# Kernel optimization log

Measured on AMD Instinct MI355X. Metric: run time of the kernel, lower is better.

Reference implementation:

```python
import jax, jax.numpy as jnp
import numpy as np

N_NODES = 50000
N_EDGES = 300000
NODE_DIM = 11
EDGE_DIM = 5
HID = 256
L = 4
G = 1024  # num graphs
BN_EPS = 1e-5


def setup_inputs() -> dict:
    key = jax.random.key(0)
    ks = jax.random.split(key, 24)
    s = 0.05
    inp = {
        "x": jax.random.normal(ks[0], (N_NODES, NODE_DIM), jnp.float32),
        "edge_index": jax.random.randint(ks[1], (2, N_EDGES), 0, N_NODES, jnp.int32),
        "edge_attr": jax.random.normal(ks[2], (N_EDGES, EDGE_DIM), jnp.float32),
        "batch": jnp.sort(jax.random.randint(ks[3], (N_NODES,), 0, G, jnp.int32)),
        # node encoder
        "enc_W": jax.random.normal(ks[4], (NODE_DIM, HID), jnp.float32) * s,
        "enc_b": jnp.zeros((HID,), jnp.float32),
        # per-layer GINE params (stacked over layers)
        "edge_W": jax.random.normal(ks[5], (L, EDGE_DIM, HID), jnp.float32) * s,
        "edge_b": jnp.zeros((L, HID), jnp.float32),
        "mlp_W1": jax.random.normal(ks[6], (L, HID, HID), jnp.float32) * s,
        "mlp_b1": jnp.zeros((L, HID), jnp.float32),
        "mlp_W2": jax.random.normal(ks[7], (L, HID, HID), jnp.float32) * s,
        "mlp_b2": jnp.zeros((L, HID), jnp.float32),
        "bn_g": jnp.ones((L, HID), jnp.float32),
        "bn_b": jnp.zeros((L, HID), jnp.float32),
        # head: 3*HID -> HID -> HID//2 -> 1
        "head_W1": jax.random.normal(ks[8], (3 * HID, HID), jnp.float32) * s,
        "head_b1": jnp.zeros((HID,), jnp.float32),
        "head_W2": jax.random.normal(ks[9], (HID, HID // 2), jnp.float32) * s,
        "head_b2": jnp.zeros((HID // 2,), jnp.float32),
        "head_W3": jax.random.normal(ks[10], (HID // 2, 1), jnp.float32) * s,
        "head_b3": jnp.zeros((1,), jnp.float32),
    }
    return inp


def _forward(x, edge_attr, enc_W, enc_b, edge_W, edge_b, mlp_W1, mlp_b1,
             mlp_W2, mlp_b2, bn_g, bn_b, head_W1, head_b1, head_W2, head_b2,
             head_W3, head_b3, edge_index, batch):
    n = x.shape[0]
    src, dst = edge_index[0], edge_index[1]  # messages flow src(j) -> dst(i)
    h = jax.nn.relu(x @ enc_W + enc_b)  # [N, HID]
    for l in range(L):
        e = edge_attr @ edge_W[l] + edge_b[l]                 # [E, HID]
        msg = jax.nn.relu(h[src] + e)                         # [E, HID]
        aggr = jax.ops.segment_sum(msg, dst, num_segments=n)  # [N, HID]
        z = h + aggr                                          # (1+eps)*h + aggr, eps=0
        z = jax.nn.relu(z @ mlp_W1[l] + mlp_b1[l]) @ mlp_W2[l] + mlp_b2[l]
        # BatchNorm over node dim (batch statistics)
        mu = jnp.mean(z, axis=0)
        var = jnp.var(z, axis=0)
        z = (z - mu) * jax.lax.rsqrt(var + BN_EPS) * bn_g[l] + bn_b[l]
        h = jax.nn.relu(z) + h  # residual
    # mean / add / max pooling per graph
    sums = jax.ops.segment_sum(h, batch, num_segments=G)      # [G, HID]
    cnt = jax.ops.segment_sum(jnp.ones((n, 1), h.dtype), batch, num_segments=G)
    mean = sums / jnp.maximum(cnt, 1.0)
    mx = jax.ops.segment_max(h, batch, num_segments=G)
    g = jnp.concatenate([mean, sums, mx], axis=1)             # [G, 3*HID]
    g = jax.nn.relu(g @ head_W1 + head_b1)
    g = jax.nn.relu(g @ head_W2 + head_b2)
    out = g @ head_W3 + head_b3
    return out.reshape(-1)  # [G]


def reference(x, edge_index, edge_attr, batch, enc_W, enc_b, edge_W, edge_b,
              mlp_W1, mlp_b1, mlp_W2, mlp_b2, bn_g, bn_b, head_W1, head_b1,
              head_W2, head_b2, head_W3, head_b3):
    return _forward(x, edge_attr, enc_W, enc_b, edge_W, edge_b, mlp_W1, mlp_b1,
                    mlp_W2, mlp_b2, bn_g, bn_b, head_W1, head_b1, head_W2,
                    head_b2, head_W3, head_b3, edge_index, batch)
```

## Files before the change

### kernel.cpp

```cpp
#include <hip/hip_runtime.h>

#define N_NODES 50000
#define N_EDGES 300000
#define G_GRAPHS 1024
#define HID 256
#define NLAYERS 4

typedef unsigned short ushort_t;
typedef __attribute__((ext_vector_type(8))) short bf16x8;
typedef __attribute__((ext_vector_type(8))) unsigned short u16x8;
typedef __attribute__((ext_vector_type(4))) float f32x4;

__device__ __forceinline__ float bf2f(ushort_t u) {
  unsigned int x = ((unsigned int)u) << 16;
  return __builtin_bit_cast(float, x);
}
__device__ __forceinline__ ushort_t f2bf(float f) {
  unsigned int x = __builtin_bit_cast(unsigned int, f);
  unsigned int lsb = (x >> 16) & 1u;
  x += 0x7fffu + lsb;
  return (ushort_t)(x >> 16);
}

__global__ __launch_bounds__(256) void k_encoder(const float* __restrict__ x,
    const float* __restrict__ W, const float* __restrict__ b,
    ushort_t* __restrict__ h, int n)
{
  int j = threadIdx.x;
  float wcol[11];
#pragma unroll
  for (int k = 0; k < 11; ++k) wcol[k] = W[k * HID + j];
  float bj = b[j];
  __shared__ float xs[8][11];
  int base = blockIdx.x * 8;
  if (j < 88) {
    int r = j / 11, k = j % 11;
    int row = base + r;
    if (row < n) xs[r][k] = x[row * 11 + k];
  }
  __syncthreads();
#pragma unroll
  for (int r = 0; r < 8; ++r) {
    int row = base + r;
    if (row >= n) break;
    float acc = bj;
#pragma unroll
    for (int k = 0; k < 11; ++k) acc += xs[r][k] * wcol[k];
    h[(size_t)row * HID + j] = f2bf(fmaxf(acc, 0.f));
  }
}

__global__ __launch_bounds__(256) void k_hist(const int* __restrict__ dst,
    int* __restrict__ offs, int E)
{
  int e = blockIdx.x * 256 + threadIdx.x;
  if (e < E) atomicAdd(&offs[dst[e]], 1);
}

__global__ __launch_bounds__(1024) void k_scanA(int* __restrict__ offs,
    int* __restrict__ btot, int n)
{
  __shared__ int wsum[16];
  int tid = threadIdx.x, lane = tid & 63, wid = tid >> 6;
  int idx = blockIdx.x * 1024 + tid;
  int v = (idx < n) ? offs[idx] : 0;
  int x = v;
#pragma unroll
  for (int off = 1; off < 64; off <<= 1) {
    int t = __shfl_up(x, off);
    if (lane >= off) x += t;
  }
  if (lane == 63) wsum[wid] = x;
  __syncthreads();
  if (wid == 0 && lane < 16) {
    int w = wsum[lane];
#pragma unroll
    for (int off = 1; off < 16; off <<= 1) {
      int t = __shfl_up(w, off);
      if (lane >= off) w += t;
    }
    wsum[lane] = w;
  }
  __syncthreads();
  int wbase = (wid == 0) ? 0 : wsum[wid - 1];
  if (idx < n) offs[idx] = wbase + x - v;
  if (tid == 0) btot[blockIdx.x] = wsum[15];
}

__global__ __launch_bounds__(1024) void k_scanC(int* __restrict__ offs,
    const int* __restrict__ btot, int n)
{
  __shared__ int sbase;
  if (threadIdx.x == 0) {
    int s = 0;
    for (int i = 0; i < blockIdx.x; ++i) s += btot[i];
    sbase = s;
  }
  __syncthreads();
  int idx = blockIdx.x * 1024 + threadIdx.x;
  if (idx < n) offs[idx] += sbase;
}

__global__ __launch_bounds__(256) void k_fill(const int* __restrict__ src,
    const int* __restrict__ dst, int* __restrict__ offs,
    int* __restrict__ esrc, ushort_t* __restrict__ eab,
    const float* __restrict__ ea, int E)
{
  int e = blockIdx.x * 256 + threadIdx.x;
  if (e < E) {
    int d = dst[e];
    int p = atomicAdd(&offs[d], 1);
    esrc[p] = src[e];
    const float* ep = ea + (size_t)e * 5;
    ushort4 lo = make_ushort4(f2bf(ep[0]), f2bf(ep[1]), f2bf(ep[2]), f2bf(ep[3]));
    ushort4 hi = make_ushort4(f2bf(ep[4]), 0, 0, 0);
    *(ushort4*)&eab[(size_t)p * 8] = lo;
    *(ushort4*)&eab[(size_t)p * 8 + 4] = hi;
  }
}

__global__ __launch_bounds__(256) void k_prep(const float* __restrict__ W1,
    const float* __restrict__ W2, ushort_t* __restrict__ Wt1,
    ushort_t* __restrict__ Wt2)
{
  __shared__ float ld[16][257];
  int mat = blockIdx.y & (NLAYERS - 1);
  int which = blockIdx.y >> 2;
  const float* Wm = (which ? W2 : W1) + (size_t)mat * HID * HID;
  ushort_t* Wtm = (which ? Wt2 : Wt1) + (size_t)mat * HID * HID;
  int k0 = blockIdx.x * 16;
  int tid = threadIdx.x;
#pragma unroll
  for (int i = 0; i < 16; ++i) ld[i][tid] = Wm[(size_t)(k0 + i) * HID + tid];
  __syncthreads();
#pragma unroll
  for (int v = 0; v < 4; ++v) {
    ushort4 u = make_ushort4(f2bf(ld[v*4+0][tid]), f2bf(ld[v*4+1][tid]),
                             f2bf(ld[v*4+2][tid]), f2bf(ld[v*4+3][tid]));
    *(ushort4*)&Wtm[(size_t)tid * HID + k0 + v * 4] = u;
  }
}

__global__ __launch_bounds__(256) void k_prept(const float* __restrict__ W,
    ushort_t* __restrict__ Wt, int K, int N)
{
  int idx = blockIdx.x * 256 + threadIdx.x;
  if (idx >= K * N) return;
  int n = idx / K, k = idx % K;
  Wt[idx] = f2bf(W[(size_t)k * N + n]);
}

struct ev5 { ushort_t s0, s1, s2, s3, s4; };

__device__ __forceinline__ void edge_step(ev5 ev, ushort4 hv,
    const float4& w0, const float4& w1, const float4& w2, const float4& w3,
    const float4& w4, const float4& bi,
    float& ax, float& ay, float& az, float& aw)
{
  float v0 = bf2f(ev.s0), v1 = bf2f(ev.s1), v2 = bf2f(ev.s2),
        v3 = bf2f(ev.s3), v4 = bf2f(ev.s4);
  float m0 = bi.x, m1 = bi.y, m2 = bi.z, m3 = bi.w;
  m0 = fmaf(v0, w0.x, m0); m1 = fmaf(v0, w0.y, m1);
  m2 = fmaf(v0, w0.z, m2); m3 = fmaf(v0, w0.w, m3);
  m0 = fmaf(v1, w1.x, m0); m1 = fmaf(v1, w1.y, m1);
  m2 = fmaf(v1, w1.z, m2); m3 = fmaf(v1, w1.w, m3);
  m0 = fmaf(v2, w2.x, m0); m1 = fmaf(v2, w2.y, m1);
  m2 = fmaf(v2, w2.z, m2); m3 = fmaf(v2, w2.w, m3);
  m0 = fmaf(v3, w3.x, m0); m1 = fmaf(v3, w3.y, m1);
  m2 = fmaf(v3, w3.z, m2); m3 = fmaf(v3, w3.w, m3);
  m0 = fmaf(v4, w4.x, m0); m1 = fmaf(v4, w4.y, m1);
  m2 = fmaf(v4, w4.z, m2); m3 = fmaf(v4, w4.w, m3);
  m0 += bf2f(hv.x); m1 += bf2f(hv.y); m2 += bf2f(hv.z); m3 += bf2f(hv.w);
  ax += fmaxf(m0, 0.f); ay += fmaxf(m1, 0.f);
  az += fmaxf(m2, 0.f); aw += fmaxf(m3, 0.f);
}

__global__ __launch_bounds__(256) void k_gather(const ushort_t* __restrict__ h,
    const int* __restrict__ offs, const int* __restrict__ esrc,
    const ushort_t* __restrict__ eab, const float* __restrict__ eW,
    const float* __restrict__ eb, ushort_t* __restrict__ zin,
    float* __restrict__ stats, int n)
{
  int tid = threadIdx.x;
  if (blockIdx.x == 0) { stats[tid] = 0.f; stats[HID + tid] = 0.f; }
  int wave = tid >> 6, lane = tid & 63;
  int node = blockIdx.x * 4 + wave;
  int c4 = lane * 4;
  float4 w0 = *(const float4*)&eW[0 * HID + c4];
  float4 w1 = *(const float4*)&eW[1 * HID + c4];
  float4 w2 = *(const float4*)&eW[2 * HID + c4];
  float4 w3 = *(const float4*)&eW[3 * HID + c4];
  float4 w4 = *(const float4*)&eW[4 * HID + c4];
  float4 bi = *(const float4*)&eb[c4];
  if (node >= n) return;
  int lo = (node == 0) ? 0 : offs[node - 1];
  int hi = offs[node];
  ushort4 ho = *(const ushort4*)&h[(size_t)node * HID + c4];
  float ax = bf2f(ho.x), ay = bf2f(ho.y), az = bf2f(ho.z), aw = bf2f(ho.w);
  int p = lo;
  for (; p + 3 < hi; p += 4) {
    int s0 = esrc[p], s1 = esrc[p + 1], s2 = esrc[p + 2], s3 = esrc[p + 3];
    ev5 ea0 = *(const ev5*)&eab[(size_t)(p + 0) * 8];
    ev5 ea1 = *(const ev5*)&eab[(size_t)(p + 1) * 8];
    ev5 ea2 = *(const ev5*)&eab[(size_t)(p + 2) * 8];
    ev5 ea3 = *(const ev5*)&eab[(size_t)(p + 3) * 8];
    ushort4 h0 = *(const ushort4*)&h[(size_t)s0 * HID + c4];
    ushort4 h1 = *(const ushort4*)&h[(size_t)s1 * HID + c4];
    ushort4 h2 = *(const ushort4*)&h[(size_t)s2 * HID + c4];
    ushort4 h3 = *(const ushort4*)&h[(size_t)s3 * HID + c4];
    edge_step(ea0, h0, w0, w1, w2, w3, w4, bi, ax, ay, az, aw);
    edge_step(ea1, h1, w0, w1, w2, w3, w4, bi, ax, ay, az, aw);
    edge_step(ea2, h2, w0, w1, w2, w3, w4, bi, ax, ay, az, aw);
    edge_step(ea3, h3, w0, w1, w2, w3, w4, bi, ax, ay, az, aw);
  }
  for (; p < hi; ++p) {
    int s0 = esrc[p];
    ev5 ea0 = *(const ev5*)&eab[(size_t)p * 8];
    ushort4 h0 = *(const ushort4*)&h[(size_t)s0 * HID + c4];
    edge_step(ea0, h0, w0, w1, w2, w3, w4, bi, ax, ay, az, aw);
  }
  *(ushort4*)&zin[(size_t)node * HID + c4] =
      make_ushort4(f2bf(ax), f2bf(ay), f2bf(az), f2bf(aw));
}

__global__ __launch_bounds__(512, 1) void k_mlp(const ushort_t* __restrict__ A,
    const ushort_t* __restrict__ Wt1, const float* __restrict__ b1,
    const ushort_t* __restrict__ Wt2, const float* __restrict__ b2,
    ushort_t* __restrict__ out, float* __restrict__ stats, int M)
{
  __shared__ alignas(16) ushort_t z1s[2][16 * 264];
  int tid = threadIdx.x;
  int wave = tid >> 6, lane = tid & 63;
  int m = lane & 15, quad = lane >> 4;
  int col0 = wave * 32;
  bf16x8 w1f[2][8];
  bf16x8 w2f[2][8];
#pragma unroll
  for (int ct = 0; ct < 2; ++ct)
#pragma unroll
    for (int kt = 0; kt < 8; ++kt) {
      w1f[ct][kt] = *(const bf16x8*)(
          Wt1 + (size_t)(col0 + ct * 16 + m) * HID + kt * 32 + quad * 8);
      w2f[ct][kt] = *(const bf16x8*)(
          Wt2 + (size_t)(col0 + ct * 16 + m) * HID + kt * 32 + quad * 8);
    }
  float bv1[2] = {b1[col0 + m], b1[col0 + 16 + m]};
  float bv2[2] = {b2[col0 + m], b2[col0 + 16 + m]};
  float csum[2] = {0.f, 0.f}, csq[2] = {0.f, 0.f};
  int ntiles = M >> 4;
  int parity = 0;
  int t = blockIdx.x;
  bf16x8 af[8];
  if (t < ntiles) {
    const ushort_t* Ap = A + (size_t)(t * 16 + m) * HID + quad * 8;
#pragma unroll
    for (int kt = 0; kt < 8; ++kt) af[kt] = *(const bf16x8*)(Ap + kt * 32);
  }
  for (; t < ntiles; t += gridDim.x) {
    int tn = t + gridDim.x;
    int tcl = (tn < ntiles) ? tn : t;
    const ushort_t* Apn = A + (size_t)(tcl * 16 + m) * HID + quad * 8;
    bf16x8 afn[8];
#pragma unroll
    for (int kt = 0; kt < 8; ++kt) afn[kt] = *(const bf16x8*)(Apn + kt * 32);
    f32x4 a0 = (f32x4){0.f, 0.f, 0.f, 0.f};
    f32x4 a1 = (f32x4){0.f, 0.f, 0.f, 0.f};
#pragma unroll
    for (int kt = 0; kt < 8; ++kt) {
      a0 = __builtin_amdgcn_mfma_f32_16x16x32_bf16(af[kt], w1f[0][kt], a0, 0, 0, 0);
      a1 = __builtin_amdgcn_mfma_f32_16x16x32_bf16(af[kt], w1f[1][kt], a1, 0, 0, 0);
    }
    ushort_t* buf = z1s[parity];
#pragma unroll
    for (int reg = 0; reg < 4; ++reg) {
      int r = quad * 4 + reg;
      buf[r * 264 + col0 + m]      = f2bf(fmaxf(a0[reg] + bv1[0], 0.f));
      buf[r * 264 + col0 + 16 + m] = f2bf(fmaxf(a1[reg] + bv1[1], 0.f));
    }
    asm volatile("s_waitcnt lgkmcnt(0)" ::: "memory");
    __builtin_amdgcn_s_barrier();
    __builtin_amdgcn_sched_barrier(0);
    f32x4 c0 = (f32x4){0.f, 0.f, 0.f, 0.f};
    f32x4 c1 = (f32x4){0.f, 0.f, 0.f, 0.f};
#pragma unroll
    for (int kt = 0; kt < 8; ++kt) {
      bf16x8 zf = *(const bf16x8*)&buf[m * 264 + kt * 32 + quad * 8];
      c0 = __builtin_amdgcn_mfma_f32_16x16x32_bf16(zf, w2f[0][kt], c0, 0, 0, 0);
      c1 = __builtin_amdgcn_mfma_f32_16x16x32_bf16(zf, w2f[1][kt], c1, 0, 0, 0);
    }
    int rb = t * 16 + quad * 4;
#pragma unroll
    for (int reg = 0; reg < 4; ++reg) {
      float o0 = c0[reg] + bv2[0];
      float o1 = c1[reg] + bv2[1];
      out[(size_t)(rb + reg) * HID + col0 + m] = f2bf(o0);
      out[(size_t)(rb + reg) * HID + col0 + 16 + m] = f2bf(o1);
      csum[0] += o0; csq[0] = fmaf(o0, o0, csq[0]);
      csum[1] += o1; csq[1] = fmaf(o1, o1, csq[1]);
    }
#pragma unroll
    for (int kt = 0; kt < 8; ++kt) af[kt] = afn[kt];
    parity ^= 1;
  }
#pragma unroll
  for (int ct = 0; ct < 2; ++ct) {
    float s = csum[ct], q = csq[ct];
    s += __shfl_xor(s, 16); s += __shfl_xor(s, 32);
    q += __shfl_xor(q, 16); q += __shfl_xor(q, 32);
    if (quad == 0) {
      unsafeAtomicAdd(&stats[col0 + ct * 16 + m], s);
      unsafeAtomicAdd(&stats[HID + col0 + ct * 16 + m], q);
    }
  }
}

__global__ __launch_bounds__(256) void k_bn_apply(const ushort_t* __restrict__ z,
    const float* __restrict__ stats, const float* __restrict__ g,
    const float* __restrict__ b, ushort_t* __restrict__ h, int total4)
{
  int idx = blockIdx.x * 256 + threadIdx.x;
  if (idx >= total4) return;
  int col = (idx & 63) * 4;
  const float inv_n = 1.f / (float)N_NODES;
  float sc[4], sh[4];
#pragma unroll
  for (int c = 0; c < 4; ++c) {
    float mu = stats[col + c] * inv_n;
    float var = stats[HID + col + c] * inv_n - mu * mu;
    float rs = rsqrtf(var + 1e-5f);
    sc[c] = g[col + c] * rs;
    sh[c] = b[col + c] - mu * sc[c];
  }
  ushort4 zv = *(const ushort4*)(z + (size_t)idx * 4);
  ushort4 hv = *(const ushort4*)(h + (size_t)idx * 4);
  float o0 = fmaxf(fmaf(bf2f(zv.x), sc[0], sh[0]), 0.f) + bf2f(hv.x);
  float o1 = fmaxf(fmaf(bf2f(zv.y), sc[1], sh[1]), 0.f) + bf2f(hv.y);
  float o2 = fmaxf(fmaf(bf2f(zv.z), sc[2], sh[2]), 0.f) + bf2f(hv.z);
  float o3 = fmaxf(fmaf(bf2f(zv.w), sc[3], sh[3]), 0.f) + bf2f(hv.w);
  *(ushort4*)(h + (size_t)idx * 4) = make_ushort4(f2bf(o0), f2bf(o1), f2bf(o2), f2bf(o3));
}

__device__ __forceinline__ int lbound(const int* __restrict__ b, int n, int key) {
  int lo = 0, hi = n;
  while (lo < hi) {
    int mid = (lo + hi) >> 1;
    if (b[mid] < key) lo = mid + 1; else hi = mid;
  }
  return lo;
}

__global__ __launch_bounds__(256) void k_pool_bn(const ushort_t* __restrict__ z,
    const float* __restrict__ stats, const float* __restrict__ g_,
    const float* __restrict__ b_, const ushort_t* __restrict__ h,
    const int* __restrict__ batch, ushort_t* __restrict__ gf)
{
  int g = blockIdx.x, j = threadIdx.x;
  const float inv_n = 1.f / (float)N_NODES;
  float mu = stats[j] * inv_n;
  float var = stats[HID + j] * inv_n - mu * mu;
  float rs = rsqrtf(var + 1e-5f);
  float sc = g_[j] * rs;
  float sh = b_[j] - mu * sc;
  int lo = lbound(batch, N_NODES, g);
  int hi = lbound(batch, N_NODES, g + 1);
  float s = 0.f, mx = 0.f;
  for (int i = lo; i < hi; ++i) {
    float zv = bf2f(z[(size_t)i * HID + j]);
    float hv = bf2f(h[(size_t)i * HID + j]);
    float v = fmaxf(fmaf(zv, sc, sh), 0.f) + hv;
    s += v; mx = fmaxf(mx, v);
  }
  float cntv = fmaxf((float)(hi - lo), 1.f);
  size_t base = (size_t)g * 768;
  gf[base + j] = f2bf(s / cntv);
  gf[base + 256 + j] = f2bf(s);
  gf[base + 512 + j] = f2bf(mx);
}

template<int KT, int DO_RELU>
__global__ __launch_bounds__(256, 1) void k_head_gemm(const ushort_t* __restrict__ A,
    const ushort_t* __restrict__ Bt, const float* __restrict__ bias,
    ushort_t* __restrict__ out, int M, int N)
{
  const int K = KT * 32;
  int tid = threadIdx.x;
  int wave = tid >> 6, lane = tid & 63;
  int m = lane & 15, quad = lane >> 4;
  int col = (blockIdx.y * 4 + wave) * 16 + m;
  bf16x8 bfrag[KT];
#pragma unroll
  for (int kt = 0; kt < KT; ++kt)
    bfrag[kt] = *(const bf16x8*)(Bt + (size_t)col * K + kt * 32 + quad * 8);
  float bv = bias[col];
  int ntiles = M >> 4;
  for (int t = blockIdx.x; t < ntiles; t += gridDim.x) {
    const ushort_t* Ap = A + (size_t)(t * 16 + m) * K + quad * 8;
    bf16x8 af[KT];
#pragma unroll
    for (int kt = 0; kt < KT; ++kt) af[kt] = *(const bf16x8*)(Ap + kt * 32);
    f32x4 acc = (f32x4){0.f, 0.f, 0.f, 0.f};
#pragma unroll
    for (int kt = 0; kt < KT; ++kt)
      acc = __builtin_amdgcn_mfma_f32_16x16x32_bf16(af[kt], bfrag[kt], acc, 0, 0, 0);
    int rb = t * 16 + quad * 4;
#pragma unroll
    for (int reg = 0; reg < 4; ++reg) {
      float o = acc[reg] + bv;
      if (DO_RELU) o = fmaxf(o, 0.f);
      out[(size_t)(rb + reg) * N + col] = f2bf(o);
    }
  }
}

__global__ __launch_bounds__(256) void k_head_out(const ushort_t* __restrict__ g2,
    const float* __restrict__ W3, const float* __restrict__ b3,
    float* __restrict__ out)
{
  int wave = threadIdx.x >> 6, lane = threadIdx.x & 63;
  int g = blockIdx.x * 4 + wave;
  ushort2 v = *(const ushort2*)&g2[(size_t)g * 128 + lane * 2];
  float p = bf2f(v.x) * W3[lane * 2] + bf2f(v.y) * W3[lane * 2 + 1];
#pragma unroll
  for (int off = 32; off > 0; off >>= 1) p += __shfl_down(p, off);
  if (lane == 0) out[g] = p + b3[0];
}

extern "C" void kernel_launch(void* const* d_in, const int* in_sizes, int n_in,
                              void* d_out, int out_size, void* d_ws, size_t ws_size,
                              hipStream_t stream)
{
  const float* x     = (const float*)d_in[0];
  const int*   ei    = (const int*)d_in[1];
  const float* ea    = (const float*)d_in[2];
  const int*   batch = (const int*)d_in[3];
  const float* encW  = (const float*)d_in[4];
  const float* encB  = (const float*)d_in[5];
  const float* edgeW = (const float*)d_in[6];
  const float* edgeB = (const float*)d_in[7];
  const float* W1    = (const float*)d_in[8];
  const float* b1    = (const float*)d_in[9];
  const float* W2    = (const float*)d_in[10];
  const float* b2    = (const float*)d_in[11];
  const float* bng   = (const float*)d_in[12];
  const float* bnb   = (const float*)d_in[13];
  const float* hW1   = (const float*)d_in[14];
  const float* hb1   = (const float*)d_in[15];
  const float* hW2   = (const float*)d_in[16];
  const float* hb2   = (const float*)d_in[17];
  const float* hW3   = (const float*)d_in[18];
  const float* hb3   = (const float*)d_in[19];
  float* out = (float*)d_out;

  const size_t NH = (size_t)N_NODES * HID;
  char* base = (char*)d_ws;
  auto alloc = [&](size_t bytes) -> char* {
    char* p = base; base += (bytes + 63) & ~(size_t)63; return p;
  };
  float*    stats = (float*)alloc(512 * 4);
  int*      offs  = (int*)alloc(50001 * 4);
  int*      btot  = (int*)alloc(64 * 4);
  int*      esrc  = (int*)alloc((size_t)N_EDGES * 4);
  ushort_t* eab   = (ushort_t*)alloc((size_t)N_EDGES * 8 * 2);
  ushort_t* Wt1   = (ushort_t*)alloc((size_t)NLAYERS * HID * HID * 2);
  ushort_t* Wt2   = (ushort_t*)alloc((size_t)NLAYERS * HID * HID * 2);
  ushort_t* hW1t  = (ushort_t*)alloc((size_t)768 * 256 * 2);
  ushort_t* hW2t  = (ushort_t*)alloc((size_t)256 * 128 * 2);
  ushort_t* gf    = (ushort_t*)alloc((size_t)G_GRAPHS * 768 * 2);
  ushort_t* g1    = (ushort_t*)alloc((size_t)G_GRAPHS * 256 * 2);
  ushort_t* g2    = (ushort_t*)alloc((size_t)G_GRAPHS * 128 * 2);
  ushort_t* zin   = (ushort_t*)alloc(NH * 2);
  ushort_t* h     = (ushort_t*)alloc(NH * 2);

  const int* src = ei;
  const int* dst = ei + N_EDGES;

  hipMemsetAsync(offs, 0, 50001 * sizeof(int), stream);
  k_hist<<<(N_EDGES + 255) / 256, 256, 0, stream>>>(dst, offs, N_EDGES);
  const int NSB = (N_NODES + 1023) / 1024;
  k_scanA<<<NSB, 1024, 0, stream>>>(offs, btot, N_NODES);
  k_scanC<<<NSB, 1024, 0, stream>>>(offs, btot, N_NODES);
  k_fill<<<(N_EDGES + 255) / 256, 256, 0, stream>>>(src, dst, offs, esrc, eab, ea, N_EDGES);
  k_prep<<<dim3(16, 2 * NLAYERS), 256, 0, stream>>>(W1, W2, Wt1, Wt2);
  k_prept<<<(768 * 256 + 255) / 256, 256, 0, stream>>>(hW1, hW1t, 768, 256);
  k_prept<<<(256 * 128 + 255) / 256, 256, 0, stream>>>(hW2, hW2t, 256, 128);

  k_encoder<<<(N_NODES + 7) / 8, 256, 0, stream>>>(x, encW, encB, h, N_NODES);

  for (int l = 0; l < NLAYERS; ++l) {
    k_gather<<<N_NODES / 4, 256, 0, stream>>>(
        h, offs, esrc, eab, edgeW + (size_t)l * 5 * HID, edgeB + (size_t)l * HID,
        zin, stats, N_NODES);
    k_mlp<<<256, 512, 0, stream>>>(
        zin, Wt1 + (size_t)l * HID * HID, b1 + (size_t)l * HID,
        Wt2 + (size_t)l * HID * HID, b2 + (size_t)l * HID, zin, stats, N_NODES);
    if (l < NLAYERS - 1) {
      k_bn_apply<<<(N_NODES * HID / 4 + 255) / 256, 256, 0, stream>>>(
          zin, stats, bng + (size_t)l * HID, bnb + (size_t)l * HID, h,
          N_NODES * HID / 4);
    }
  }

  k_pool_bn<<<G_GRAPHS, 256, 0, stream>>>(
      zin, stats, bng + (size_t)(NLAYERS - 1) * HID,
      bnb + (size_t)(NLAYERS - 1) * HID, h, batch, gf);
  k_head_gemm<24, 1><<<dim3(16, 4), 256, 0, stream>>>(gf, hW1t, hb1, g1, G_GRAPHS, 256);
  k_head_gemm<8, 1><<<dim3(16, 2), 256, 0, stream>>>(g1, hW2t, hb2, g2, G_GRAPHS, 128);
  k_head_out<<<G_GRAPHS / 4, 256, 0, stream>>>(g2, hW3, hb3, out);
}
```

Before: 602.9 us.

## Pad CSR segments to multiples of four and pipeline gather over four-node groups

```diff
diff --git a/kernel.cpp b/kernel.cpp
--- a/kernel.cpp
+++ b/kernel.cpp
@@ -5,6 +5,7 @@
 #define G_GRAPHS 1024
 #define HID 256
 #define NLAYERS 4
+#define PAD_SLOTS (N_EDGES + 3 * N_NODES + 64)
 
 typedef unsigned short ushort_t;
 typedef __attribute__((ext_vector_type(8))) short bf16x8;
@@ -63,7 +64,8 @@
   __shared__ int wsum[16];
   int tid = threadIdx.x, lane = tid & 63, wid = tid >> 6;
   int idx = blockIdx.x * 1024 + tid;
-  int v = (idx < n) ? offs[idx] : 0;
+  int cnt = (idx < n) ? offs[idx] : 0;
+  int v = (cnt + 3) & ~3;
   int x = v;
 #pragma unroll
   for (int off = 1; off < 64; off <<= 1) {
@@ -88,17 +90,22 @@
 }
 
 __global__ __launch_bounds__(1024) void k_scanC(int* __restrict__ offs,
-    const int* __restrict__ btot, int n)
+    int* __restrict__ pstart, const int* __restrict__ btot, int n)
 {
   __shared__ int sbase;
   if (threadIdx.x == 0) {
     int s = 0;
-    for (int i = 0; i < blockIdx.x; ++i) s += btot[i];
+    for (int i = 0; i < (int)blockIdx.x; ++i) s += btot[i];
     sbase = s;
+    if (blockIdx.x == gridDim.x - 1) pstart[n] = s + btot[blockIdx.x];
   }
   __syncthreads();
   int idx = blockIdx.x * 1024 + threadIdx.x;
-  if (idx < n) offs[idx] += sbase;
+  if (idx < n) {
+    int v = offs[idx] + sbase;
+    offs[idx] = v;
+    pstart[idx] = v;
+  }
 }
 
 __global__ __launch_bounds__(256) void k_fill(const int* __restrict__ src,
@@ -113,7 +120,7 @@
     esrc[p] = src[e];
     const float* ep = ea + (size_t)e * 5;
     ushort4 lo = make_ushort4(f2bf(ep[0]), f2bf(ep[1]), f2bf(ep[2]), f2bf(ep[3]));
-    ushort4 hi = make_ushort4(f2bf(ep[4]), 0, 0, 0);
+    ushort4 hi = make_ushort4(f2bf(ep[4]), (ushort_t)0x3f80u, 0, 0);
     *(ushort4*)&eab[(size_t)p * 8] = lo;
     *(ushort4*)&eab[(size_t)p * 8 + 4] = hi;
   }
@@ -150,15 +157,14 @@
   Wt[idx] = f2bf(W[(size_t)k * N + n]);
 }
 
-struct ev5 { ushort_t s0, s1, s2, s3, s4; };
-
-__device__ __forceinline__ void edge_step(ev5 ev, ushort4 hv,
+__device__ __forceinline__ void edge_step(bf16x8 ev, ushort4 hv,
     const float4& w0, const float4& w1, const float4& w2, const float4& w3,
     const float4& w4, const float4& bi,
     float& ax, float& ay, float& az, float& aw)
 {
-  float v0 = bf2f(ev.s0), v1 = bf2f(ev.s1), v2 = bf2f(ev.s2),
-        v3 = bf2f(ev.s3), v4 = bf2f(ev.s4);
+  float v0 = bf2f((ushort_t)ev[0]), v1 = bf2f((ushort_t)ev[1]),
+        v2 = bf2f((ushort_t)ev[2]), v3 = bf2f((ushort_t)ev[3]),
+        v4 = bf2f((ushort_t)ev[4]), fl = bf2f((ushort_t)ev[5]);
   float m0 = bi.x, m1 = bi.y, m2 = bi.z, m3 = bi.w;
   m0 = fmaf(v0, w0.x, m0); m1 = fmaf(v0, w0.y, m1);
   m2 = fmaf(v0, w0.z, m2); m3 = fmaf(v0, w0.w, m3);
@@ -171,12 +177,14 @@
   m0 = fmaf(v4, w4.x, m0); m1 = fmaf(v4, w4.y, m1);
   m2 = fmaf(v4, w4.z, m2); m3 = fmaf(v4, w4.w, m3);
   m0 += bf2f(hv.x); m1 += bf2f(hv.y); m2 += bf2f(hv.z); m3 += bf2f(hv.w);
-  ax += fmaxf(m0, 0.f); ay += fmaxf(m1, 0.f);
-  az += fmaxf(m2, 0.f); aw += fmaxf(m3, 0.f);
+  ax = fmaf(fl, fmaxf(m0, 0.f), ax);
+  ay = fmaf(fl, fmaxf(m1, 0.f), ay);
+  az = fmaf(fl, fmaxf(m2, 0.f), az);
+  aw = fmaf(fl, fmaxf(m3, 0.f), aw);
 }
 
 __global__ __launch_bounds__(256) void k_gather(const ushort_t* __restrict__ h,
-    const int* __restrict__ offs, const int* __restrict__ esrc,
+    const int* __restrict__ pstart, const int* __restrict__ esrc,
     const ushort_t* __restrict__ eab, const float* __restrict__ eW,
     const float* __restrict__ eb, ushort_t* __restrict__ zin,
     float* __restrict__ stats, int n)
@@ -184,7 +192,6 @@
   int tid = threadIdx.x;
   if (blockIdx.x == 0) { stats[tid] = 0.f; stats[HID + tid] = 0.f; }
   int wave = tid >> 6, lane = tid & 63;
-  int node = blockIdx.x * 4 + wave;
   int c4 = lane * 4;
   float4 w0 = *(const float4*)&eW[0 * HID + c4];
   float4 w1 = *(const float4*)&eW[1 * HID + c4];
@@ -192,35 +199,67 @@
   float4 w3 = *(const float4*)&eW[3 * HID + c4];
   float4 w4 = *(const float4*)&eW[4 * HID + c4];
   float4 bi = *(const float4*)&eb[c4];
-  if (node >= n) return;
-  int lo = (node == 0) ? 0 : offs[node - 1];
-  int hi = offs[node];
-  ushort4 ho = *(const ushort4*)&h[(size_t)node * HID + c4];
-  float ax = bf2f(ho.x), ay = bf2f(ho.y), az = bf2f(ho.z), aw = bf2f(ho.w);
-  int p = lo;
-  for (; p + 3 < hi; p += 4) {
-    int s0 = esrc[p], s1 = esrc[p + 1], s2 = esrc[p + 2], s3 = esrc[p + 3];
-    ev5 ea0 = *(const ev5*)&eab[(size_t)(p + 0) * 8];
-    ev5 ea1 = *(const ev5*)&eab[(size_t)(p + 1) * 8];
-    ev5 ea2 = *(const ev5*)&eab[(size_t)(p + 2) * 8];
-    ev5 ea3 = *(const ev5*)&eab[(size_t)(p + 3) * 8];
-    ushort4 h0 = *(const ushort4*)&h[(size_t)s0 * HID + c4];
-    ushort4 h1 = *(const ushort4*)&h[(size_t)s1 * HID + c4];
-    ushort4 h2 = *(const ushort4*)&h[(size_t)s2 * HID + c4];
-    ushort4 h3 = *(const ushort4*)&h[(size_t)s3 * HID + c4];
-    edge_step(ea0, h0, w0, w1, w2, w3, w4, bi, ax, ay, az, aw);
-    edge_step(ea1, h1, w0, w1, w2, w3, w4, bi, ax, ay, az, aw);
-    edge_step(ea2, h2, w0, w1, w2, w3, w4, bi, ax, ay, az, aw);
-    edge_step(ea3, h3, w0, w1, w2, w3, w4, bi, ax, ay, az, aw);
-  }
-  for (; p < hi; ++p) {
-    int s0 = esrc[p];
-    ev5 ea0 = *(const ev5*)&eab[(size_t)p * 8];
-    ushort4 h0 = *(const ushort4*)&h[(size_t)s0 * HID + c4];
-    edge_step(ea0, h0, w0, w1, w2, w3, w4, bi, ax, ay, az, aw);
-  }
-  *(ushort4*)&zin[(size_t)node * HID + c4] =
-      make_ushort4(f2bf(ax), f2bf(ay), f2bf(az), f2bf(aw));
+  int n0 = (blockIdx.x * 4 + wave) * 4;
+  if (n0 >= n) return;
+  int e0 = __builtin_amdgcn_readfirstlane(pstart[n0]);
+  int e1 = __builtin_amdgcn_readfirstlane(pstart[n0 + 1]);
+  int e2 = __builtin_amdgcn_readfirstlane(pstart[n0 + 2]);
+  int e3 = __builtin_amdgcn_readfirstlane(pstart[n0 + 3]);
+  int e4 = __builtin_amdgcn_readfirstlane(pstart[n0 + 4]);
+  float A[4][4];
+#pragma unroll
+  for (int j = 0; j < 4; ++j) {
+    ushort4 hv = *(const ushort4*)&h[(size_t)(n0 + j) * HID + c4];
+    A[j][0] = bf2f(hv.x); A[j][1] = bf2f(hv.y);
+    A[j][2] = bf2f(hv.z); A[j][3] = bf2f(hv.w);
+  }
+  int p = e0, pend = e4;
+  bf16x8 ec0, ec1, ec2, ec3;
+  ushort4 hc0, hc1, hc2, hc3;
+  int sn0, sn1, sn2, sn3;
+  if (p < pend) {
+    int sc0 = esrc[p], sc1 = esrc[p + 1], sc2 = esrc[p + 2], sc3 = esrc[p + 3];
+    ec0 = *(const bf16x8*)&eab[(size_t)(p + 0) * 8];
+    ec1 = *(const bf16x8*)&eab[(size_t)(p + 1) * 8];
+    ec2 = *(const bf16x8*)&eab[(size_t)(p + 2) * 8];
+    ec3 = *(const bf16x8*)&eab[(size_t)(p + 3) * 8];
+    hc0 = *(const ushort4*)&h[(size_t)sc0 * HID + c4];
+    hc1 = *(const ushort4*)&h[(size_t)sc1 * HID + c4];
+    hc2 = *(const ushort4*)&h[(size_t)sc2 * HID + c4];
+    hc3 = *(const ushort4*)&h[(size_t)sc3 * HID + c4];
+    int pn = (p + 4 < pend) ? p + 4 : p;
+    sn0 = esrc[pn]; sn1 = esrc[pn + 1]; sn2 = esrc[pn + 2]; sn3 = esrc[pn + 3];
+  }
+  for (; p < pend; p += 4) {
+    int pn = (p + 4 < pend) ? p + 4 : p;
+    int pnn = (p + 8 < pend) ? p + 8 : p;
+    bf16x8 en0 = *(const bf16x8*)&eab[(size_t)(pn + 0) * 8];
+    bf16x8 en1 = *(const bf16x8*)&eab[(size_t)(pn + 1) * 8];
+    bf16x8 en2 = *(const bf16x8*)&eab[(size_t)(pn + 2) * 8];
+    bf16x8 en3 = *(const bf16x8*)&eab[(size_t)(pn + 3) * 8];
+    ushort4 hn0 = *(const ushort4*)&h[(size_t)sn0 * HID + c4];
+    ushort4 hn1 = *(const ushort4*)&h[(size_t)sn1 * HID + c4];
+    ushort4 hn2 = *(const ushort4*)&h[(size_t)sn2 * HID + c4];
+    ushort4 hn3 = *(const ushort4*)&h[(size_t)sn3 * HID + c4];
+    int sm0 = esrc[pnn], sm1 = esrc[pnn + 1], sm2 = esrc[pnn + 2], sm3 = esrc[pnn + 3];
+    float c0 = 0.f, c1 = 0.f, c2 = 0.f, c3 = 0.f;
+    edge_step(ec0, hc0, w0, w1, w2, w3, w4, bi, c0, c1, c2, c3);
+    edge_step(ec1, hc1, w0, w1, w2, w3, w4, bi, c0, c1, c2, c3);
+    edge_step(ec2, hc2, w0, w1, w2, w3, w4, bi, c0, c1, c2, c3);
+    edge_step(ec3, hc3, w0, w1, w2, w3, w4, bi, c0, c1, c2, c3);
+    if (p < e1)      { A[0][0] += c0; A[0][1] += c1; A[0][2] += c2; A[0][3] += c3; }
+    else if (p < e2) { A[1][0] += c0; A[1][1] += c1; A[1][2] += c2; A[1][3] += c3; }
+    else if (p < e3) { A[2][0] += c0; A[2][1] += c1; A[2][2] += c2; A[2][3] += c3; }
+    else             { A[3][0] += c0; A[3][1] += c1; A[3][2] += c2; A[3][3] += c3; }
+    ec0 = en0; ec1 = en1; ec2 = en2; ec3 = en3;
+    hc0 = hn0; hc1 = hn1; hc2 = hn2; hc3 = hn3;
+    sn0 = sm0; sn1 = sm1; sn2 = sm2; sn3 = sm3;
+  }
+#pragma unroll
+  for (int j = 0; j < 4; ++j) {
+    *(ushort4*)&zin[(size_t)(n0 + j) * HID + c4] =
+        make_ushort4(f2bf(A[j][0]), f2bf(A[j][1]), f2bf(A[j][2]), f2bf(A[j][3]));
+  }
 }
 
 __global__ __launch_bounds__(512, 1) void k_mlp(const ushort_t* __restrict__ A,
@@ -458,9 +497,10 @@
   };
   float*    stats = (float*)alloc(512 * 4);
   int*      offs  = (int*)alloc(50001 * 4);
+  int*      pstart= (int*)alloc(50001 * 4);
   int*      btot  = (int*)alloc(64 * 4);
-  int*      esrc  = (int*)alloc((size_t)N_EDGES * 4);
-  ushort_t* eab   = (ushort_t*)alloc((size_t)N_EDGES * 8 * 2);
+  int*      esrc  = (int*)alloc((size_t)PAD_SLOTS * 4);
+  ushort_t* eab   = (ushort_t*)alloc((size_t)PAD_SLOTS * 8 * 2);
   ushort_t* Wt1   = (ushort_t*)alloc((size_t)NLAYERS * HID * HID * 2);
   ushort_t* Wt2   = (ushort_t*)alloc((size_t)NLAYERS * HID * HID * 2);
   ushort_t* hW1t  = (ushort_t*)alloc((size_t)768 * 256 * 2);
@@ -475,10 +515,12 @@
   const int* dst = ei + N_EDGES;
 
   hipMemsetAsync(offs, 0, 50001 * sizeof(int), stream);
+  hipMemsetAsync(esrc, 0, (size_t)PAD_SLOTS * 4, stream);
+  hipMemsetAsync(eab, 0, (size_t)PAD_SLOTS * 16, stream);
   k_hist<<<(N_EDGES + 255) / 256, 256, 0, stream>>>(dst, offs, N_EDGES);
   const int NSB = (N_NODES + 1023) / 1024;
   k_scanA<<<NSB, 1024, 0, stream>>>(offs, btot, N_NODES);
-  k_scanC<<<NSB, 1024, 0, stream>>>(offs, btot, N_NODES);
+  k_scanC<<<NSB, 1024, 0, stream>>>(offs, pstart, btot, N_NODES);
   k_fill<<<(N_EDGES + 255) / 256, 256, 0, stream>>>(src, dst, offs, esrc, eab, ea, N_EDGES);
   k_prep<<<dim3(16, 2 * NLAYERS), 256, 0, stream>>>(W1, W2, Wt1, Wt2);
   k_prept<<<(768 * 256 + 255) / 256, 256, 0, stream>>>(hW1, hW1t, 768, 256);
@@ -487,8 +529,8 @@
   k_encoder<<<(N_NODES + 7) / 8, 256, 0, stream>>>(x, encW, encB, h, N_NODES);
 
   for (int l = 0; l < NLAYERS; ++l) {
-    k_gather<<<N_NODES / 4, 256, 0, stream>>>(
-        h, offs, esrc, eab, edgeW + (size_t)l * 5 * HID, edgeB + (size_t)l * HID,
+    k_gather<<<(N_NODES + 15) / 16, 256, 0, stream>>>(
+        h, pstart, esrc, eab, edgeW + (size_t)l * 5 * HID, edgeB + (size_t)l * HID,
         zin, stats, N_NODES);
     k_mlp<<<256, 512, 0, stream>>>(
         zin, Wt1 + (size_t)l * HID * HID, b1 + (size_t)l * HID,
```

Result: faster. 574.1 us (-4.8%).
